# Kernel tuning notes

Measured on AMD Instinct MI355X. Metric: run time of the kernel, lower is better.

## Reference

```python
import jax, jax.numpy as jnp
import numpy as np

N_EMBED = 1024
HEAD_SIZE = 128
B, T = 8, 2048

def setup_inputs() -> dict:
    key = jax.random.key(0)
    kx, kq, kk, kv = jax.random.split(key, 4)
    x = jax.random.normal(kx, (B, T, N_EMBED), dtype=jnp.float32)
    s = N_EMBED ** -0.5
    Wq = jax.random.normal(kq, (N_EMBED, HEAD_SIZE), dtype=jnp.float32) * s
    Wk = jax.random.normal(kk, (N_EMBED, HEAD_SIZE), dtype=jnp.float32) * s
    Wv = jax.random.normal(kv, (N_EMBED, HEAD_SIZE), dtype=jnp.float32) * s
    return {"x": x, "Wq": Wq, "Wk": Wk, "Wv": Wv}

def reference(x, Wq, Wk, Wv):
    # x: [B, T, C]; single causal attention head, eval mode (dropout = identity).
    Bb, Tt, C = x.shape
    q = x @ Wq  # [B, T, H]
    k = x @ Wk  # [B, T, H]
    v = x @ Wv  # [B, T, H]
    # NOTE: original scales by C**-0.5 with C = n_embed (input dim), not head_size.
    wgt = jnp.einsum('bqh,bkh->bqk', q, k) * (C ** -0.5)  # [B, T, T]
    causal = jnp.tril(jnp.ones((Tt, Tt), dtype=bool))
    wgt = jnp.where(causal, wgt, -jnp.inf)
    wgt = jax.nn.softmax(wgt, axis=-1)
    return wgt @ v  # [B, T, H]
```

## Files before the change

kernel.cpp:

```cpp
#include <hip/hip_runtime.h>
#include <hip/hip_bf16.h>

#define B_  8
#define T_  2048
#define C_  1024
#define H_  128

using f32x4  = __attribute__((ext_vector_type(4))) float;
using f32x16 = __attribute__((ext_vector_type(16))) float;
using bf16x8 = __attribute__((ext_vector_type(8))) short;

__device__ __forceinline__ unsigned short f2bf(float f) {
    union { float f; unsigned u; } v; v.f = f;
    unsigned r = v.u + 0x7FFFu + ((v.u >> 16) & 1u);
    return (unsigned short)(r >> 16);
}
__device__ __forceinline__ float bf2f(unsigned short s) {
    union { unsigned u; float f; } v; v.u = ((unsigned)s) << 16;
    return v.f;
}

#define BAR() do { asm volatile("s_waitcnt lgkmcnt(0)" ::: "memory"); \
                   __builtin_amdgcn_s_barrier(); } while (0)

template<int C>
__device__ __forceinline__ float dppf(float v) {
    return __int_as_float(__builtin_amdgcn_update_dpp(0, __float_as_int(v), C, 0xF, 0xF, true));
}
#define DPPRED_MAX(v) { v = fmaxf(v, dppf<0xB1>(v)); v = fmaxf(v, dppf<0x4E>(v)); \
                        v = fmaxf(v, dppf<0x141>(v)); v = fmaxf(v, dppf<0x140>(v)); }
#define DPPRED_SUM(v) { v = v + dppf<0xB1>(v); v = v + dppf<0x4E>(v); \
                        v = v + dppf<0x141>(v); v = v + dppf<0x140>(v); }

__global__ void wconv_kernel(const float* __restrict__ Wq,
                             const float* __restrict__ Wk,
                             const float* __restrict__ Wv,
                             unsigned short* __restrict__ Wt) {
    int id  = blockIdx.x * 256 + threadIdx.x;
    int col = id % 384;
    int k   = id / 384;
    const float* W = (col < 128) ? Wq : ((col < 256) ? Wk : Wv);
    float v = W[k * H_ + (col & 127)];
    if (col < 128) v *= 0.03125f;
    Wt[(size_t)(k >> 5) * 12288 + col * 32 + (k & 31)] = f2bf(v);
}

__launch_bounds__(512, 2)
__global__ void gemm_kernel(const float* __restrict__ x,
                            const unsigned short* __restrict__ Wt,
                            unsigned short* __restrict__ qb,
                            unsigned short* __restrict__ kb,
                            unsigned short* __restrict__ vT) {
    __shared__ unsigned short Bs[2][13824];
    __shared__ unsigned short As[2][2304];

    const int tid  = threadIdx.x;
    const int wave = tid >> 6;
    const int lane = tid & 63;
    const int r32 = lane & 31, hi32 = lane >> 5;
    const int row0 = blockIdx.x * 64;
    const int wrow  = (wave >> 2) * 32;
    const int wcol0 = (wave & 3) * 96;

    const int arow = tid >> 3;
    const int ak4  = (tid & 7) * 4;
    const float* xsrc = x + (size_t)(row0 + arow) * C_ + ak4;
    const unsigned short* bsrc = Wt + (size_t)tid * 8;

    f32x16 acc[3];
    #pragma unroll
    for (int ct = 0; ct < 3; ++ct)
        #pragma unroll
        for (int e = 0; e < 16; ++e) acc[ct][e] = 0.f;

    {
        #pragma unroll
        for (int j = 0; j < 3; ++j) {
            const int chunk = tid + j * 512;
            *(uint4*)&Bs[0][(chunk >> 2) * 36 + (chunk & 3) * 8] =
                *(const uint4*)(bsrc + j * 4096);
        }
        float4 f = *(const float4*)(xsrc);
        unsigned a0 = f2bf(f.x) | ((unsigned)f2bf(f.y) << 16);
        unsigned a1 = f2bf(f.z) | ((unsigned)f2bf(f.w) << 16);
        *(uint2*)&As[0][arow * 36 + ak4] = uint2{a0, a1};
    }
    float4 hA = *(const float4*)(xsrc + 32);
    float4 hB = *(const float4*)(xsrc + 64);
    BAR();

    for (int k = 0; k < 32; ++k) {
        const int cur = k & 1, nxt = cur ^ 1;

        uint4 br[3];
        float4 xf;
        if (k < 31) {
            const unsigned short* g = bsrc + (size_t)(k + 1) * 12288;
            #pragma unroll
            for (int j = 0; j < 3; ++j) br[j] = *(const uint4*)(g + j * 4096);
        }
        {
            const int kn = (k + 3 < 31) ? k + 3 : 31;
            xf = *(const float4*)(xsrc + kn * 32);
        }

        #pragma unroll
        for (int kh = 0; kh < 2; ++kh) {
            const int kofs = kh * 16 + 8 * hi32;
            bf16x8 af = *(const bf16x8*)&As[cur][(wrow + r32) * 36 + kofs];
            #pragma unroll
            for (int ct = 0; ct < 3; ++ct) {
                bf16x8 bf = *(const bf16x8*)&Bs[cur][(wcol0 + ct * 32 + r32) * 36 + kofs];
                acc[ct] = __builtin_amdgcn_mfma_f32_32x32x16_bf16(af, bf, acc[ct], 0, 0, 0);
            }
        }

        if (k < 31) {
            #pragma unroll
            for (int j = 0; j < 3; ++j) {
                const int chunk = tid + j * 512;
                *(uint4*)&Bs[nxt][(chunk >> 2) * 36 + (chunk & 3) * 8] = br[j];
            }
            unsigned a0 = f2bf(hA.x) | ((unsigned)f2bf(hA.y) << 16);
            unsigned a1 = f2bf(hA.z) | ((unsigned)f2bf(hA.w) << 16);
            *(uint2*)&As[nxt][arow * 36 + ak4] = uint2{a0, a1};
        }
        BAR();
        hA = hB; hB = xf;
    }

    #pragma unroll
    for (int ct = 0; ct < 3; ++ct) {
        int col = wcol0 + ct * 32 + r32;
        int head = col >> 7;
        int h = col & 127;
        #pragma unroll
        for (int reg = 0; reg < 16; ++reg) {
            int rg = row0 + wrow + (reg & 3) + 8 * (reg >> 2) + 4 * hi32;
            unsigned short val = f2bf(acc[ct][reg]);
            if (head == 0)      qb[(size_t)rg * H_ + h] = val;
            else if (head == 1) kb[(size_t)rg * H_ + h] = val;
            else {
                int b = rg >> 11, t = rg & (T_ - 1);
                vT[((size_t)b * H_ + h) * T_ + t] = val;
            }
        }
    }
}

__launch_bounds__(512, 2)
__global__ void attn1_kernel(const unsigned short* __restrict__ qb,
                             const unsigned short* __restrict__ kb,
                             const unsigned short* __restrict__ vT,
                             unsigned short* __restrict__ Opart,
                             float* __restrict__ MLpart) {
    __shared__ unsigned short Ks[2][64 * 128];
    __shared__ unsigned short Vs[2][128 * 64];
    __shared__ unsigned short Ps[8][16][72];

    const int tid  = threadIdx.x;
    const int wave = tid >> 6;
    const int lane = tid & 63;
    const int lo = lane & 15, hi = lane >> 4;

    const int bid   = blockIdx.x;
    const int b     = bid & 7;
    const int chunk = (bid >> 3) & 7;
    const int qt    = 7 - (bid >> 6);
    if (chunk > qt) return;

    const int kv_begin = chunk << 8;
    const size_t bT = (size_t)b * T_;
    const int qrow0 = (qt << 8) + wave * 32;

    const int krow = tid >> 3, kcol = (tid & 7) * 2;
    const int vrow = tid >> 2, vcol = (tid & 3) * 2;
    const unsigned short* kgsrc = kb + (bT + krow) * H_ + kcol * 8;
    const unsigned short* vgsrc = vT + ((size_t)b * H_ + vrow) * T_ + vcol * 8;
    const int koff0 = krow * 128 + ((kcol ^ (krow & 7)) * 8);
    const int koff1 = krow * 128 + (((kcol + 1) ^ (krow & 7)) * 8);
    const int voff0 = vrow * 64 + ((vcol ^ (vrow & 7)) * 8);
    const int voff1 = vrow * 64 + (((vcol + 1) ^ (vrow & 7)) * 8);

    bf16x8 qf[2][4];
    #pragma unroll
    for (int q2 = 0; q2 < 2; ++q2)
        #pragma unroll
        for (int kc = 0; kc < 4; ++kc)
            qf[q2][kc] = *(const bf16x8*)(qb + (bT + qrow0 + 16 * q2 + lo) * H_ + kc * 32 + 8 * hi);

    float m[2][4], l[2][4];
    f32x4 o[2][8];
    #pragma unroll
    for (int q2 = 0; q2 < 2; ++q2)
        #pragma unroll
        for (int r = 0; r < 4; ++r) { m[q2][r] = -1e30f; l[q2][r] = 0.f; }
    #pragma unroll
    for (int q2 = 0; q2 < 2; ++q2)
        #pragma unroll
        for (int ct = 0; ct < 8; ++ct) o[q2][ct] = f32x4{0.f, 0.f, 0.f, 0.f};

    {
        uint4 a = *(const uint4*)(kgsrc + (size_t)kv_begin * H_);
        uint4 c = *(const uint4*)(kgsrc + (size_t)kv_begin * H_ + 8);
        uint4 d = *(const uint4*)(vgsrc + kv_begin);
        uint4 e = *(const uint4*)(vgsrc + kv_begin + 8);
        *(uint4*)&Ks[0][koff0] = a;
        *(uint4*)&Ks[0][koff1] = c;
        *(uint4*)&Vs[0][voff0] = d;
        *(uint4*)&Vs[0][voff1] = e;
    }
    uint4 kr0 = *(const uint4*)(kgsrc + (size_t)(kv_begin + 64) * H_);
    uint4 kr1 = *(const uint4*)(kgsrc + (size_t)(kv_begin + 64) * H_ + 8);
    uint4 vr0 = *(const uint4*)(vgsrc + kv_begin + 64);
    uint4 vr1 = *(const uint4*)(vgsrc + kv_begin + 64 + 8);
    BAR();

    for (int t = 0; t < 4; ++t) {
        const int cur = t & 1;
        const int kv0 = kv_begin + t * 64;

        if (kv0 <= qrow0 + 31) {
            f32x4 s[2][4];
            #pragma unroll
            for (int q2 = 0; q2 < 2; ++q2)
                #pragma unroll
                for (int ct4 = 0; ct4 < 4; ++ct4) s[q2][ct4] = f32x4{0.f, 0.f, 0.f, 0.f};
            __builtin_amdgcn_s_setprio(1);
            #pragma unroll
            for (int ct4 = 0; ct4 < 4; ++ct4) {
                const int row = ct4 * 16 + lo;
                #pragma unroll
                for (int kc = 0; kc < 4; ++kc) {
                    bf16x8 kf = *(const bf16x8*)&Ks[cur][row * 128 + (((kc * 4 + hi) ^ (row & 7)) * 8)];
                    s[0][ct4] = __builtin_amdgcn_mfma_f32_16x16x32_bf16(qf[0][kc], kf, s[0][ct4], 0, 0, 0);
                    s[1][ct4] = __builtin_amdgcn_mfma_f32_16x16x32_bf16(qf[1][kc], kf, s[1][ct4], 0, 0, 0);
                }
            }
            __builtin_amdgcn_s_setprio(0);

            if (kv0 + 63 >= qrow0) {
                #pragma unroll
                for (int q2 = 0; q2 < 2; ++q2)
                    #pragma unroll
                    for (int ct4 = 0; ct4 < 4; ++ct4)
                        #pragma unroll
                        for (int r = 0; r < 4; ++r)
                            if (kv0 + ct4 * 16 + lo > qrow0 + 16 * q2 + 4 * hi + r)
                                s[q2][ct4][r] = -1e30f;
            }

            float alpha[2][4];
            #pragma unroll
            for (int q2 = 0; q2 < 2; ++q2) {
                #pragma unroll
                for (int r = 0; r < 4; ++r) {
                    float pm = fmaxf(fmaxf(s[q2][0][r], s[q2][1][r]), fmaxf(s[q2][2][r], s[q2][3][r]));
                    DPPRED_MAX(pm);
                    float mn = fmaxf(m[q2][r], pm);
                    alpha[q2][r] = __expf(m[q2][r] - mn);
                    m[q2][r] = mn;
                    #pragma unroll
                    for (int ct4 = 0; ct4 < 4; ++ct4) s[q2][ct4][r] = __expf(s[q2][ct4][r] - mn);
                    float rs = (s[q2][0][r] + s[q2][1][r]) + (s[q2][2][r] + s[q2][3][r]);
                    DPPRED_SUM(rs);
                    l[q2][r] = l[q2][r] * alpha[q2][r] + rs;
                }
            }
            #pragma unroll
            for (int q2 = 0; q2 < 2; ++q2)
                #pragma unroll
                for (int ct = 0; ct < 8; ++ct)
                    #pragma unroll
                    for (int r = 0; r < 4; ++r) o[q2][ct][r] *= alpha[q2][r];

            bf16x8 pa[2][2];
            #pragma unroll
            for (int q2 = 0; q2 < 2; ++q2) {
                #pragma unroll
                for (int ct4 = 0; ct4 < 4; ++ct4)
                    #pragma unroll
                    for (int r = 0; r < 4; ++r)
                        Ps[wave][4 * hi + r][ct4 * 16 + lo] = f2bf(s[q2][ct4][r]);
                pa[q2][0] = *(const bf16x8*)&Ps[wave][lo][8 * hi];
                pa[q2][1] = *(const bf16x8*)&Ps[wave][lo][32 + 8 * hi];
            }

            __builtin_amdgcn_s_setprio(1);
            #pragma unroll
            for (int ct = 0; ct < 8; ++ct) {
                const int row = ct * 16 + lo;
                #pragma unroll
                for (int half = 0; half < 2; ++half) {
                    bf16x8 vf = *(const bf16x8*)&Vs[cur][row * 64 + (((half * 4 + hi) ^ (row & 7)) * 8)];
                    o[0][ct] = __builtin_amdgcn_mfma_f32_16x16x32_bf16(pa[0][half], vf, o[0][ct], 0, 0, 0);
                    o[1][ct] = __builtin_amdgcn_mfma_f32_16x16x32_bf16(pa[1][half], vf, o[1][ct], 0, 0, 0);
                }
            }
            __builtin_amdgcn_s_setprio(0);
        }

        if (t < 3) {
            *(uint4*)&Ks[cur ^ 1][koff0] = kr0;
            *(uint4*)&Ks[cur ^ 1][koff1] = kr1;
            *(uint4*)&Vs[cur ^ 1][voff0] = vr0;
            *(uint4*)&Vs[cur ^ 1][voff1] = vr1;
            if (t < 2) {
                const int kvn = kv_begin + (t + 2) * 64;
                kr0 = *(const uint4*)(kgsrc + (size_t)kvn * H_);
                kr1 = *(const uint4*)(kgsrc + (size_t)kvn * H_ + 8);
                vr0 = *(const uint4*)(vgsrc + kvn);
                vr1 = *(const uint4*)(vgsrc + kvn + 8);
            }
        }
        BAR();
    }

    const int slot = b * 36 + ((qt * (qt + 1)) >> 1) + chunk;
    unsigned short* op = Opart + (size_t)slot * 32768 + (size_t)(wave * 32) * 128;
    #pragma unroll
    for (int q2 = 0; q2 < 2; ++q2)
        #pragma unroll
        for (int ct = 0; ct < 8; ++ct)
            #pragma unroll
            for (int r = 0; r < 4; ++r)
                op[(16 * q2 + 4 * hi + r) * 128 + ct * 16 + lo] = f2bf(o[q2][ct][r]);
    if (lo == 0) {
        #pragma unroll
        for (int q2 = 0; q2 < 2; ++q2)
            #pragma unroll
            for (int r = 0; r < 4; ++r) {
                int base = slot * 512 + (wave * 32 + 16 * q2 + 4 * hi + r) * 2;
                MLpart[base]     = m[q2][r];
                MLpart[base + 1] = l[q2][r];
            }
    }
}

__launch_bounds__(128)
__global__ void attn2_kernel(const unsigned short* __restrict__ Opart,
                             const float* __restrict__ MLpart,
                             float* __restrict__ out) {
    const int bid = blockIdx.x;
    const int b   = bid & 7;
    const int qt  = (bid >> 3) & 7;
    const int sub = bid >> 6;
    const int nch = qt + 1;
    const int slot0 = b * 36 + ((qt * (qt + 1)) >> 1);

    const int tid  = threadIdx.x;
    const int row  = tid >> 2;
    const int h0   = (tid & 3) * 32;
    const int srow = sub * 32 + row;

    float M = -1e30f;
    for (int c = 0; c < nch; ++c)
        M = fmaxf(M, MLpart[(slot0 + c) * 512 + srow * 2]);
    float L = 0.f;
    for (int c = 0; c < nch; ++c) {
        float mc = MLpart[(slot0 + c) * 512 + srow * 2];
        float lc = MLpart[(slot0 + c) * 512 + srow * 2 + 1];
        L += lc * __expf(mc - M);
    }

    float accv[32];
    #pragma unroll
    for (int j = 0; j < 32; ++j) accv[j] = 0.f;
    for (int c = 0; c < nch; ++c) {
        float wc = __expf(MLpart[(slot0 + c) * 512 + srow * 2] - M);
        const unsigned short* src = Opart + (size_t)(slot0 + c) * 32768 + (size_t)srow * 128 + h0;
        #pragma unroll
        for (int j = 0; j < 4; ++j) {
            bf16x8 v = *(const bf16x8*)(src + j * 8);
            #pragma unroll
            for (int e = 0; e < 8; ++e)
                accv[j * 8 + e] += wc * bf2f((unsigned short)v[e]);
        }
    }
    float inv = 1.f / L;
    float4* dst = (float4*)(out + ((size_t)b * T_ + qt * 256 + srow) * H_ + h0);
    #pragma unroll
    for (int j = 0; j < 8; ++j)
        dst[j] = float4{accv[4 * j] * inv, accv[4 * j + 1] * inv,
                        accv[4 * j + 2] * inv, accv[4 * j + 3] * inv};
}

extern "C" void kernel_launch(void* const* d_in, const int* in_sizes, int n_in,
                              void* d_out, int out_size, void* d_ws, size_t ws_size,
                              hipStream_t stream) {
    const float* x  = (const float*)d_in[0];
    const float* Wq = (const float*)d_in[1];
    const float* Wk = (const float*)d_in[2];
    const float* Wv = (const float*)d_in[3];
    float* out = (float*)d_out;

    char* ws = (char*)d_ws;
    unsigned short* Wt  = (unsigned short*)ws;
    unsigned short* qbf = (unsigned short*)(ws + (size_t)384 * 1024 * 2);
    unsigned short* kbf = qbf + (size_t)B_ * T_ * H_;
    unsigned short* vTf = kbf + (size_t)B_ * T_ * H_;
    unsigned short* Opart = vTf + (size_t)B_ * T_ * H_;
    float* MLpart = (float*)((char*)Opart + (size_t)288 * 32768 * 2);

    wconv_kernel<<<(384 * 1024) / 256, 256, 0, stream>>>(Wq, Wk, Wv, Wt);
    gemm_kernel<<<B_ * T_ / 64, 512, 0, stream>>>(x, Wt, qbf, kbf, vTf);
    attn1_kernel<<<512, 512, 0, stream>>>(qbf, kbf, vTf, Opart, MLpart);
    attn2_kernel<<<512, 128, 0, stream>>>(Opart, MLpart, out);
}
```

Before: 86.31 us.

## Halve GEMM block to 4 waves with 2x3 MFMA tiles per wave

The QKV projection GEMM now uses 256 threads per block instead of 512. Each wave computes two 32-row tiles across three 32-column tiles, so every B fragment read from LDS feeds two MFMAs. This cuts LDS reads per MFMA and barrier overhead per unit of work. In exchange each thread carries twice the accumulators and staging loads, and the launch bound drops to (256,1), which may lower occupancy and latency hiding.

```diff
diff --git a/kernel.cpp b/kernel.cpp
--- a/kernel.cpp
+++ b/kernel.cpp
@@ -45,7 +45,7 @@
     Wt[(size_t)(k >> 5) * 12288 + col * 32 + (k & 31)] = f2bf(v);
 }
 
-__launch_bounds__(512, 2)
+__launch_bounds__(256, 1)
 __global__ void gemm_kernel(const float* __restrict__ x,
                             const unsigned short* __restrict__ Wt,
                             unsigned short* __restrict__ qb,
@@ -58,91 +58,106 @@
     const int wave = tid >> 6;
     const int lane = tid & 63;
     const int r32 = lane & 31, hi32 = lane >> 5;
-    const int row0 = blockIdx.x * 64;
-    const int wrow  = (wave >> 2) * 32;
-    const int wcol0 = (wave & 3) * 96;
-
-    const int arow = tid >> 3;
-    const int ak4  = (tid & 7) * 4;
-    const float* xsrc = x + (size_t)(row0 + arow) * C_ + ak4;
+    const int row0  = blockIdx.x * 64;
+    const int wcol0 = wave * 96;
+
+    const int arow = tid >> 2;
+    const int aq8  = (tid & 3) * 8;
+    const float* xsrc = x + (size_t)(row0 + arow) * C_ + aq8;
+
     const unsigned short* bsrc = Wt + (size_t)tid * 8;
 
-    f32x16 acc[3];
-    #pragma unroll
-    for (int ct = 0; ct < 3; ++ct)
-        #pragma unroll
-        for (int e = 0; e < 16; ++e) acc[ct][e] = 0.f;
+    f32x16 acc[2][3];
+    #pragma unroll
+    for (int rt = 0; rt < 2; ++rt)
+        #pragma unroll
+        for (int ct = 0; ct < 3; ++ct)
+            #pragma unroll
+            for (int e = 0; e < 16; ++e) acc[rt][ct][e] = 0.f;
 
     {
         #pragma unroll
-        for (int j = 0; j < 3; ++j) {
-            const int chunk = tid + j * 512;
+        for (int j = 0; j < 6; ++j) {
+            const int chunk = tid + j * 256;
             *(uint4*)&Bs[0][(chunk >> 2) * 36 + (chunk & 3) * 8] =
-                *(const uint4*)(bsrc + j * 4096);
-        }
-        float4 f = *(const float4*)(xsrc);
-        unsigned a0 = f2bf(f.x) | ((unsigned)f2bf(f.y) << 16);
-        unsigned a1 = f2bf(f.z) | ((unsigned)f2bf(f.w) << 16);
-        *(uint2*)&As[0][arow * 36 + ak4] = uint2{a0, a1};
-    }
-    float4 hA = *(const float4*)(xsrc + 32);
-    float4 hB = *(const float4*)(xsrc + 64);
+                *(const uint4*)(bsrc + j * 2048);
+        }
+        float4 f0 = *(const float4*)(xsrc);
+        float4 f1 = *(const float4*)(xsrc + 4);
+        unsigned a0 = f2bf(f0.x) | ((unsigned)f2bf(f0.y) << 16);
+        unsigned a1 = f2bf(f0.z) | ((unsigned)f2bf(f0.w) << 16);
+        unsigned a2 = f2bf(f1.x) | ((unsigned)f2bf(f1.y) << 16);
+        unsigned a3 = f2bf(f1.z) | ((unsigned)f2bf(f1.w) << 16);
+        *(uint4*)&As[0][arow * 36 + aq8] = uint4{a0, a1, a2, a3};
+    }
+    float4 hA0 = *(const float4*)(xsrc + 32);
+    float4 hA1 = *(const float4*)(xsrc + 36);
+    float4 hB0 = *(const float4*)(xsrc + 64);
+    float4 hB1 = *(const float4*)(xsrc + 68);
     BAR();
 
     for (int k = 0; k < 32; ++k) {
         const int cur = k & 1, nxt = cur ^ 1;
 
-        uint4 br[3];
-        float4 xf;
+        uint4 br[6];
         if (k < 31) {
             const unsigned short* g = bsrc + (size_t)(k + 1) * 12288;
             #pragma unroll
-            for (int j = 0; j < 3; ++j) br[j] = *(const uint4*)(g + j * 4096);
-        }
-        {
-            const int kn = (k + 3 < 31) ? k + 3 : 31;
-            xf = *(const float4*)(xsrc + kn * 32);
-        }
+            for (int j = 0; j < 6; ++j) br[j] = *(const uint4*)(g + j * 2048);
+        }
+        const int kn = (k + 3 < 31) ? k + 3 : 31;
+        float4 xf0 = *(const float4*)(xsrc + kn * 32);
+        float4 xf1 = *(const float4*)(xsrc + kn * 32 + 4);
 
         #pragma unroll
         for (int kh = 0; kh < 2; ++kh) {
             const int kofs = kh * 16 + 8 * hi32;
-            bf16x8 af = *(const bf16x8*)&As[cur][(wrow + r32) * 36 + kofs];
+            bf16x8 af[2];
+            #pragma unroll
+            for (int rt = 0; rt < 2; ++rt)
+                af[rt] = *(const bf16x8*)&As[cur][(rt * 32 + r32) * 36 + kofs];
             #pragma unroll
             for (int ct = 0; ct < 3; ++ct) {
                 bf16x8 bf = *(const bf16x8*)&Bs[cur][(wcol0 + ct * 32 + r32) * 36 + kofs];
-                acc[ct] = __builtin_amdgcn_mfma_f32_32x32x16_bf16(af, bf, acc[ct], 0, 0, 0);
+                #pragma unroll
+                for (int rt = 0; rt < 2; ++rt)
+                    acc[rt][ct] = __builtin_amdgcn_mfma_f32_32x32x16_bf16(af[rt], bf, acc[rt][ct], 0, 0, 0);
             }
         }
 
         if (k < 31) {
             #pragma unroll
-            for (int j = 0; j < 3; ++j) {
-                const int chunk = tid + j * 512;
+            for (int j = 0; j < 6; ++j) {
+                const int chunk = tid + j * 256;
                 *(uint4*)&Bs[nxt][(chunk >> 2) * 36 + (chunk & 3) * 8] = br[j];
             }
-            unsigned a0 = f2bf(hA.x) | ((unsigned)f2bf(hA.y) << 16);
-            unsigned a1 = f2bf(hA.z) | ((unsigned)f2bf(hA.w) << 16);
-            *(uint2*)&As[nxt][arow * 36 + ak4] = uint2{a0, a1};
+            unsigned a0 = f2bf(hA0.x) | ((unsigned)f2bf(hA0.y) << 16);
+            unsigned a1 = f2bf(hA0.z) | ((unsigned)f2bf(hA0.w) << 16);
+            unsigned a2 = f2bf(hA1.x) | ((unsigned)f2bf(hA1.y) << 16);
+            unsigned a3 = f2bf(hA1.z) | ((unsigned)f2bf(hA1.w) << 16);
+            *(uint4*)&As[nxt][arow * 36 + aq8] = uint4{a0, a1, a2, a3};
         }
         BAR();
-        hA = hB; hB = xf;
-    }
-
-    #pragma unroll
-    for (int ct = 0; ct < 3; ++ct) {
-        int col = wcol0 + ct * 32 + r32;
-        int head = col >> 7;
-        int h = col & 127;
-        #pragma unroll
-        for (int reg = 0; reg < 16; ++reg) {
-            int rg = row0 + wrow + (reg & 3) + 8 * (reg >> 2) + 4 * hi32;
-            unsigned short val = f2bf(acc[ct][reg]);
-            if (head == 0)      qb[(size_t)rg * H_ + h] = val;
-            else if (head == 1) kb[(size_t)rg * H_ + h] = val;
-            else {
-                int b = rg >> 11, t = rg & (T_ - 1);
-                vT[((size_t)b * H_ + h) * T_ + t] = val;
+        hA0 = hB0; hA1 = hB1; hB0 = xf0; hB1 = xf1;
+    }
+
+    #pragma unroll
+    for (int rt = 0; rt < 2; ++rt) {
+        #pragma unroll
+        for (int ct = 0; ct < 3; ++ct) {
+            int col = wcol0 + ct * 32 + r32;
+            int head = col >> 7;
+            int h = col & 127;
+            #pragma unroll
+            for (int reg = 0; reg < 16; ++reg) {
+                int rg = row0 + rt * 32 + (reg & 3) + 8 * (reg >> 2) + 4 * hi32;
+                unsigned short val = f2bf(acc[rt][ct][reg]);
+                if (head == 0)      qb[(size_t)rg * H_ + h] = val;
+                else if (head == 1) kb[(size_t)rg * H_ + h] = val;
+                else {
+                    int b = rg >> 11, t = rg & (T_ - 1);
+                    vT[((size_t)b * H_ + h) * T_ + t] = val;
+                }
             }
         }
     }
@@ -403,7 +418,7 @@
     float* MLpart = (float*)((char*)Opart + (size_t)288 * 32768 * 2);
 
     wconv_kernel<<<(384 * 1024) / 256, 256, 0, stream>>>(Wq, Wk, Wv, Wt);
-    gemm_kernel<<<B_ * T_ / 64, 512, 0, stream>>>(x, Wt, qbf, kbf, vTf);
+    gemm_kernel<<<B_ * T_ / 64, 256, 0, stream>>>(x, Wt, qbf, kbf, vTf);
     attn1_kernel<<<512, 512, 0, stream>>>(qbf, kbf, vTf, Opart, MLpart);
     attn2_kernel<<<512, 128, 0, stream>>>(Opart, MLpart, out);
 }
```

Result: slower. 130.2 us (+50.9%).

## Rewrite QKV projection GEMM to load operands directly from global, dropping LDS staging

Applied to the files above, without the earlier changes.

The projection GEMM no longer stages x and weight tiles through double-buffered shared memory with barriers. Each wave now loads its MFMA fragments straight from global memory with one-step register prefetch and converts fp32 x to bf16 using packed cvt instructions. Blocks shrink to 32 rows and 6 waves of 64 columns, so there are more blocks and no LDS or barrier overhead. In exchange, x is re-read by every wave (6x redundancy) and weight fragments by every block, which relies on L2/L1 caching and may raise global traffic.

```diff
diff --git a/kernel.cpp b/kernel.cpp
--- a/kernel.cpp
+++ b/kernel.cpp
@@ -18,6 +18,15 @@
 __device__ __forceinline__ float bf2f(unsigned short s) {
     union { unsigned u; float f; } v; v.u = ((unsigned)s) << 16;
     return v.f;
+}
+
+__device__ __forceinline__ bf16x8 cvt8(float4 f0, float4 f1) {
+    union { unsigned u[4]; bf16x8 v; } r;
+    asm("v_cvt_pk_bf16_f32 %0, %1, %2" : "=v"(r.u[0]) : "v"(f0.x), "v"(f0.y));
+    asm("v_cvt_pk_bf16_f32 %0, %1, %2" : "=v"(r.u[1]) : "v"(f0.z), "v"(f0.w));
+    asm("v_cvt_pk_bf16_f32 %0, %1, %2" : "=v"(r.u[2]) : "v"(f1.x), "v"(f1.y));
+    asm("v_cvt_pk_bf16_f32 %0, %1, %2" : "=v"(r.u[3]) : "v"(f1.z), "v"(f1.w));
+    return r.v;
 }
 
 #define BAR() do { asm volatile("s_waitcnt lgkmcnt(0)" ::: "memory"); \
@@ -45,98 +54,70 @@
     Wt[(size_t)(k >> 5) * 12288 + col * 32 + (k & 31)] = f2bf(v);
 }
 
-__launch_bounds__(512, 2)
+__launch_bounds__(384, 3)
 __global__ void gemm_kernel(const float* __restrict__ x,
                             const unsigned short* __restrict__ Wt,
                             unsigned short* __restrict__ qb,
                             unsigned short* __restrict__ kb,
                             unsigned short* __restrict__ vT) {
-    __shared__ unsigned short Bs[2][13824];
-    __shared__ unsigned short As[2][2304];
-
     const int tid  = threadIdx.x;
     const int wave = tid >> 6;
     const int lane = tid & 63;
     const int r32 = lane & 31, hi32 = lane >> 5;
-    const int row0 = blockIdx.x * 64;
-    const int wrow  = (wave >> 2) * 32;
-    const int wcol0 = (wave & 3) * 96;
-
-    const int arow = tid >> 3;
-    const int ak4  = (tid & 7) * 4;
-    const float* xsrc = x + (size_t)(row0 + arow) * C_ + ak4;
-    const unsigned short* bsrc = Wt + (size_t)tid * 8;
-
-    f32x16 acc[3];
-    #pragma unroll
-    for (int ct = 0; ct < 3; ++ct)
+    const int row0  = blockIdx.x * 32;
+    const int wcol0 = wave * 64;
+
+    const float* xa = x + (size_t)(row0 + r32) * C_ + hi32 * 8;
+    const unsigned short* wb = Wt + (size_t)(wcol0 + r32) * 32 + hi32 * 8;
+
+    f32x16 acc[2];
+    #pragma unroll
+    for (int ct = 0; ct < 2; ++ct)
         #pragma unroll
         for (int e = 0; e < 16; ++e) acc[ct][e] = 0.f;
 
-    {
-        #pragma unroll
-        for (int j = 0; j < 3; ++j) {
-            const int chunk = tid + j * 512;
-            *(uint4*)&Bs[0][(chunk >> 2) * 36 + (chunk & 3) * 8] =
-                *(const uint4*)(bsrc + j * 4096);
-        }
-        float4 f = *(const float4*)(xsrc);
-        unsigned a0 = f2bf(f.x) | ((unsigned)f2bf(f.y) << 16);
-        unsigned a1 = f2bf(f.z) | ((unsigned)f2bf(f.w) << 16);
-        *(uint2*)&As[0][arow * 36 + ak4] = uint2{a0, a1};
-    }
-    float4 hA = *(const float4*)(xsrc + 32);
-    float4 hB = *(const float4*)(xsrc + 64);
-    BAR();
-
+    float4 a00 = *(const float4*)(xa);
+    float4 a01 = *(const float4*)(xa + 4);
+    float4 a10 = *(const float4*)(xa + 16);
+    float4 a11 = *(const float4*)(xa + 20);
+    bf16x8 b00 = *(const bf16x8*)(wb);
+    bf16x8 b01 = *(const bf16x8*)(wb + 16);
+    bf16x8 b10 = *(const bf16x8*)(wb + 1024);
+    bf16x8 b11 = *(const bf16x8*)(wb + 1024 + 16);
+
+    #pragma unroll 2
     for (int k = 0; k < 32; ++k) {
-        const int cur = k & 1, nxt = cur ^ 1;
-
-        uint4 br[3];
-        float4 xf;
-        if (k < 31) {
-            const unsigned short* g = bsrc + (size_t)(k + 1) * 12288;
-            #pragma unroll
-            for (int j = 0; j < 3; ++j) br[j] = *(const uint4*)(g + j * 4096);
-        }
-        {
-            const int kn = (k + 3 < 31) ? k + 3 : 31;
-            xf = *(const float4*)(xsrc + kn * 32);
-        }
-
-        #pragma unroll
-        for (int kh = 0; kh < 2; ++kh) {
-            const int kofs = kh * 16 + 8 * hi32;
-            bf16x8 af = *(const bf16x8*)&As[cur][(wrow + r32) * 36 + kofs];
-            #pragma unroll
-            for (int ct = 0; ct < 3; ++ct) {
-                bf16x8 bf = *(const bf16x8*)&Bs[cur][(wcol0 + ct * 32 + r32) * 36 + kofs];
-                acc[ct] = __builtin_amdgcn_mfma_f32_32x32x16_bf16(af, bf, acc[ct], 0, 0, 0);
-            }
-        }
-
-        if (k < 31) {
-            #pragma unroll
-            for (int j = 0; j < 3; ++j) {
-                const int chunk = tid + j * 512;
-                *(uint4*)&Bs[nxt][(chunk >> 2) * 36 + (chunk & 3) * 8] = br[j];
-            }
-            unsigned a0 = f2bf(hA.x) | ((unsigned)f2bf(hA.y) << 16);
-            unsigned a1 = f2bf(hA.z) | ((unsigned)f2bf(hA.w) << 16);
-            *(uint2*)&As[nxt][arow * 36 + ak4] = uint2{a0, a1};
-        }
-        BAR();
-        hA = hB; hB = xf;
-    }
-
-    #pragma unroll
-    for (int ct = 0; ct < 3; ++ct) {
+        const int kn = (k + 1 < 32) ? k + 1 : 31;
+        const float* xp = xa + kn * 32;
+        const unsigned short* wp = wb + (size_t)kn * 12288;
+        float4 n00 = *(const float4*)(xp);
+        float4 n01 = *(const float4*)(xp + 4);
+        float4 n10 = *(const float4*)(xp + 16);
+        float4 n11 = *(const float4*)(xp + 20);
+        bf16x8 c00 = *(const bf16x8*)(wp);
+        bf16x8 c01 = *(const bf16x8*)(wp + 16);
+        bf16x8 c10 = *(const bf16x8*)(wp + 1024);
+        bf16x8 c11 = *(const bf16x8*)(wp + 1024 + 16);
+
+        bf16x8 aC0 = cvt8(a00, a01);
+        bf16x8 aC1 = cvt8(a10, a11);
+        acc[0] = __builtin_amdgcn_mfma_f32_32x32x16_bf16(aC0, b00, acc[0], 0, 0, 0);
+        acc[1] = __builtin_amdgcn_mfma_f32_32x32x16_bf16(aC0, b10, acc[1], 0, 0, 0);
+        acc[0] = __builtin_amdgcn_mfma_f32_32x32x16_bf16(aC1, b01, acc[0], 0, 0, 0);
+        acc[1] = __builtin_amdgcn_mfma_f32_32x32x16_bf16(aC1, b11, acc[1], 0, 0, 0);
+
+        a00 = n00; a01 = n01; a10 = n10; a11 = n11;
+        b00 = c00; b01 = c01; b10 = c10; b11 = c11;
+    }
+
+    #pragma unroll
+    for (int ct = 0; ct < 2; ++ct) {
         int col = wcol0 + ct * 32 + r32;
         int head = col >> 7;
         int h = col & 127;
         #pragma unroll
         for (int reg = 0; reg < 16; ++reg) {
-            int rg = row0 + wrow + (reg & 3) + 8 * (reg >> 2) + 4 * hi32;
+            int rg = row0 + (reg & 3) + 8 * (reg >> 2) + 4 * hi32;
             unsigned short val = f2bf(acc[ct][reg]);
             if (head == 0)      qb[(size_t)rg * H_ + h] = val;
             else if (head == 1) kb[(size_t)rg * H_ + h] = val;
@@ -403,7 +384,7 @@
     float* MLpart = (float*)((char*)Opart + (size_t)288 * 32768 * 2);
 
     wconv_kernel<<<(384 * 1024) / 256, 256, 0, stream>>>(Wq, Wk, Wv, Wt);
-    gemm_kernel<<<B_ * T_ / 64, 512, 0, stream>>>(x, Wt, qbf, kbf, vTf);
+    gemm_kernel<<<B_ * T_ / 32, 384, 0, stream>>>(x, Wt, qbf, kbf, vTf);
     attn1_kernel<<<512, 512, 0, stream>>>(qbf, kbf, vTf, Opart, MLpart);
     attn2_kernel<<<512, 128, 0, stream>>>(Opart, MLpart, out);
 }
```

Result: slower. 129.2 us (+49.7%).
